# Performance work log

Hardware: AMD Instinct MI355X
Metric: run time of the kernel (lower is better)

Reference implementation:

```python
import jax, jax.numpy as jnp
import numpy as np

N, D, V = 4096, 256, 32000
B, T = 32, 256
U_DECAY, X_DECAY = 0.97, 0.97
EPS = 1e-6


def layernorm_row(z):
    # matches torch: (z - mean) / (std + eps), std with Bessel correction (ddof=1)
    m = jnp.mean(z, axis=-1, keepdims=True)
    s = jnp.std(z, axis=-1, keepdims=True, ddof=1)
    return (z - m) / (s + EPS)


def setup_inputs() -> dict:
    key = jax.random.key(0)
    k1, k2, k3, k4, k5 = jax.random.split(key, 5)
    token_emb = jax.random.normal(k1, (V, D), jnp.float32) / np.float32(np.sqrt(D))
    E = jax.random.normal(k2, (D, N), jnp.float32) / np.float32(np.sqrt(N))
    Dx = jax.random.normal(k3, (N, D), jnp.float32) / np.float32(np.sqrt(D))
    Dy = jax.random.normal(k4, (N, D), jnp.float32) / np.float32(np.sqrt(D))
    idx = jax.random.randint(k5, (B, T), 0, V)
    return {"idx": idx, "token_emb": token_emb, "E": E, "Dx": Dx, "Dy": Dy}


def reference(idx, token_emb, E, Dx, Dy):
    b = idx.shape[0]

    def step(carry, tok):
        x, rho = carry                                   # x: (b,n), rho: (b,d,n)
        v_prev = token_emb[tok]                          # (b,d) embedding gather
        x_t = X_DECAY * x + jax.nn.relu(v_prev @ Dx.T)   # (b,n)
        x_t = x_t / (jnp.sum(jnp.abs(x_t), axis=-1, keepdims=True) + EPS)  # L1 normalize
        a_star = jnp.einsum('bdn,bn->bd', rho, x_t)      # fast-weight readout
        y_t = jax.nn.relu(layernorm_row(a_star) @ Dy.T) * jax.nn.relu(x_t)  # (b,n)
        v_star = layernorm_row(y_t @ E.T)                # (b,d)
        # Hebbian decayed outer-product memory update
        rho = U_DECAY * (rho + jnp.einsum('bd,bn->bdn', layernorm_row(v_prev), x_t))
        return (x_t, rho), v_star

    x0 = jnp.zeros((b, N), jnp.float32)
    rho0 = jnp.zeros((b, D, N), jnp.float32)
    (_, _), vs = jax.lax.scan(step, (x0, rho0), idx.T)   # vs: (T,b,d)
    return jnp.transpose(vs, (1, 0, 2))                  # (b,T,d)
```

## Files before the change

### kernel.cpp

```cpp
#include <hip/hip_runtime.h>
#include <hip/hip_bf16.h>

#define NN 4096
#define DD 256
#define BB 32
#define TT 256
#define EPS 1e-6f
#define DECAY 0.97f
#define LOG2_DECAY -0.043943348f

typedef __hip_bfloat16 bf16;
typedef short short8 __attribute__((ext_vector_type(8)));
typedef float floatx4 __attribute__((ext_vector_type(4)));

__device__ __forceinline__ float bfu2f(short u) {
    return __uint_as_float(((unsigned)(unsigned short)u) << 16);
}
__device__ __forceinline__ short f2bfu(float v) {
    bf16 t = __float2bfloat16(v);
    return *reinterpret_cast<short*>(&t);
}

__device__ __forceinline__ float blk_sum_256(float v, volatile float* s4) {
#pragma unroll
    for (int o = 32; o > 0; o >>= 1) v += __shfl_down(v, o, 64);
    int lane = threadIdx.x & 63, w = threadIdx.x >> 6;
    __syncthreads();
    if (lane == 0) s4[w] = v;
    __syncthreads();
    return s4[0] + s4[1] + s4[2] + s4[3];
}

__device__ __forceinline__ void gl16(const bf16* g, void* l) {
    __builtin_amdgcn_global_load_lds((const __attribute__((address_space(1))) void*)g,
                                     (__attribute__((address_space(3))) void*)l, 16, 0, 0);
}

__device__ __forceinline__ short8 frag(const char* matbase, int row, int c) {
    return *(const short8*)(matbase + row * 128 + (((c) ^ (row & 7)) << 4));
}

__global__ void k_detect(const unsigned short* __restrict__ raw, int* __restrict__ flag) {
    __shared__ int cnt[4];
    int tid = threadIdx.x;
    int bad = 0;
    for (int i = tid; i < 8192; i += 256) {
        unsigned int u = raw[2 * i];
        float v = __uint_as_float(u << 16);
        if (!(fabsf(v) < 1e6f)) bad++;
    }
#pragma unroll
    for (int o = 32; o > 0; o >>= 1) bad += __shfl_down(bad, o, 64);
    int lane = tid & 63, w = tid >> 6;
    if (lane == 0) cnt[w] = bad;
    __syncthreads();
    if (tid == 0) flag[0] = (cnt[0] + cnt[1] + cnt[2] + cnt[3] < 32) ? 1 : 0;
}

__global__ __launch_bounds__(256) void k_convert3(const void* __restrict__ s0,
                                                  const void* __restrict__ s1,
                                                  const void* __restrict__ s2,
                                                  bf16* __restrict__ d0,
                                                  bf16* __restrict__ d1,
                                                  bf16* __restrict__ d2,
                                                  const int* __restrict__ flag) {
    const int per = NN * DD / 8;
    int i = blockIdx.x * 256 + threadIdx.x;
    int m = i / per, j = i % per;
    const void* s = (m == 0) ? s0 : (m == 1) ? s1 : s2;
    bf16* d = (m == 0) ? d0 : (m == 1) ? d1 : d2;
    if (flag[0]) {
        ((uint4*)d)[j] = ((const uint4*)s)[j];
    } else {
        const float4* f = (const float4*)s;
        float4 a = f[2 * j], b = f[2 * j + 1];
        short8 o;
        float va[8] = {a.x, a.y, a.z, a.w, b.x, b.y, b.z, b.w};
#pragma unroll
        for (int k = 0; k < 8; k++) o[k] = f2bfu(va[k]);
        ((short8*)d)[j] = o;
    }
}

__global__ __launch_bounds__(256) void k_gather_ln(const void* __restrict__ emb,
                                                   const int* __restrict__ idx,
                                                   bf16* __restrict__ Vpb,
                                                   bf16* __restrict__ Ub,
                                                   const int* __restrict__ flag) {
    __shared__ float s4[4];
    int r = blockIdx.x, d = threadIdx.x;
    int tok = idx[r];
    long o = (long)tok * DD + d;
    float e = flag[0] ? __bfloat162float(((const bf16*)emb)[o]) : ((const float*)emb)[o];
    Vpb[(long)r * DD + d] = __float2bfloat16(e);
    float m = blk_sum_256(e, s4) * (1.0f / DD);
    float zc = e - m;
    float var = blk_sum_256(zc * zc, s4) * (1.0f / (DD - 1));
    Ub[(long)r * DD + d] = __float2bfloat16(zc / (sqrtf(fmaxf(var, 0.f)) + EPS));
}

__global__ __launch_bounds__(256) void k_transpose(const bf16* __restrict__ Ub,
                                                   bf16* __restrict__ Ut) {
    __shared__ bf16 tile[32][33];
    int b = blockIdx.z;
    int t0 = blockIdx.x * 32, d0 = blockIdx.y * 32;
    const bf16* src = Ub + (long)b * TT * DD;
    bf16* dst = Ut + (long)b * DD * TT;
    int rr = threadIdx.x >> 3, c4 = (threadIdx.x & 7) * 4;
#pragma unroll
    for (int i = 0; i < 4; i++) tile[rr][c4 + i] = src[(long)(t0 + rr) * DD + d0 + c4 + i];
    __syncthreads();
#pragma unroll
    for (int i = 0; i < 4; i++) dst[(long)(d0 + rr) * TT + t0 + c4 + i] = tile[c4 + i][rr];
}

enum { EPI_RELU_BF16 = 0, EPI_RELU_MULX_BF16 = 2 };

template <int EPI>
__global__ __launch_bounds__(256) void k_g128(const bf16* __restrict__ A,
                                              const bf16* __restrict__ B,
                                              bf16* __restrict__ C,
                                              const bf16* __restrict__ Xaux,
                                              float* __restrict__ Wsum) {
    __shared__ __align__(16) char smem[65536];
    const int lda = DD, ldb = DD, ldc = NN;
    int bm = blockIdx.y * 128, bn = blockIdx.x * 128;
    int tid = threadIdx.x, w = tid >> 6, lane = tid & 63;
    int lrow = lane >> 3, lph = lane & 7;
    int rr0 = w * 32;
    int csw = lph ^ lrow;

    floatx4 acc[4][4];
#pragma unroll
    for (int i = 0; i < 4; i++)
#pragma unroll
        for (int j = 0; j < 4; j++) acc[i][j] = (floatx4){0.f, 0.f, 0.f, 0.f};

#define STAGE128(buf, k0)                                                              \
    {                                                                                  \
        char* bb = smem + (buf)*32768;                                                 \
        _Pragma("unroll") for (int j = 0; j < 4; j++) {                                \
            int row = rr0 + j * 8 + lrow;                                              \
            gl16(A + (long)(bm + row) * lda + (k0) + csw * 8,                          \
                 bb + (rr0 + j * 8) * 128 + lane * 16);                                \
            gl16(B + (long)(bn + row) * ldb + (k0) + csw * 8,                          \
                 bb + 16384 + (rr0 + j * 8) * 128 + lane * 16);                        \
        }                                                                              \
    }

    int wm = (w >> 1) * 64, wn = (w & 1) * 64;
    int lm = lane & 15, kh = lane >> 4;

    STAGE128(0, 0);
#pragma unroll
    for (int it = 0; it < 4; it++) {
        __syncthreads();
        if (it < 3) STAGE128((it + 1) & 1, (it + 1) * 64);
        char* Ab = smem + (it & 1) * 32768;
        char* Bb = Ab + 16384;
#pragma unroll
        for (int ks = 0; ks < 2; ks++) {
            int c = ks * 4 + kh;
            short8 af[4], bfr[4];
#pragma unroll
            for (int i = 0; i < 4; i++) af[i] = frag(Ab, wm + i * 16 + lm, c);
#pragma unroll
            for (int j = 0; j < 4; j++) bfr[j] = frag(Bb, wn + j * 16 + lm, c);
#pragma unroll
            for (int i = 0; i < 4; i++)
#pragma unroll
                for (int j = 0; j < 4; j++)
                    acc[i][j] = __builtin_amdgcn_mfma_f32_16x16x32_bf16(af[i], bfr[j], acc[i][j], 0, 0, 0);
        }
    }
#undef STAGE128

    bf16* R = (bf16*)smem;
#pragma unroll
    for (int p = 0; p < 2; p++) {
        __syncthreads();
        if ((w >> 1) == p) {
#pragma unroll
            for (int i = 0; i < 4; i++)
#pragma unroll
                for (int j = 0; j < 4; j++)
#pragma unroll
                    for (int r = 0; r < 4; r++) {
                        int rr = i * 16 + kh * 4 + r;
                        int cc = wn + j * 16 + lm;
                        R[rr * 136 + cc] = __float2bfloat16(fmaxf(acc[i][j][r], 0.f));
                    }
        }
        __syncthreads();
#pragma unroll
        for (int it2 = 0; it2 < 4; it2++) {
            int row_l = it2 * 16 + (tid >> 4);
            int c8 = (tid & 15) * 8;
            short8 vv = *(const short8*)(R + row_l * 136 + c8);
            int gm = bm + p * 64 + row_l;
            long off = (long)gm * ldc + bn + c8;
            if (EPI == EPI_RELU_BF16) {
                *(short8*)(C + off) = vv;
                float s = 0.f;
#pragma unroll
                for (int k = 0; k < 8; k++) s += bfu2f(vv[k]);
#pragma unroll
                for (int o = 8; o > 0; o >>= 1) s += __shfl_down(s, o, 16);
                if ((tid & 15) == 0) atomicAdd(&Wsum[gm], s);
            } else {
                short8 xx = *(const short8*)(Xaux + off);
                short8 oo;
#pragma unroll
                for (int k = 0; k < 8; k++) oo[k] = f2bfu(bfu2f(vv[k]) * fmaxf(bfu2f(xx[k]), 0.f));
                *(short8*)(C + off) = oo;
            }
        }
    }
}

template <int KITERS>
__global__ __launch_bounds__(256) void k_g64x128(const bf16* __restrict__ A, int lda, long sA,
                                                 const bf16* __restrict__ B, int ldb, long sB,
                                                 float* __restrict__ C, int ldc, long sC) {
    __shared__ __align__(16) char smem[49152];
    int z = blockIdx.z;
    A += (long)z * sA;
    B += (long)z * sB;
    long cbase = (long)z * sC;
    int bm = blockIdx.y * 64, bn = blockIdx.x * 128;
    int tid = threadIdx.x, w = tid >> 6, lane = tid & 63;
    int lrow = lane >> 3, lph = lane & 7;
    int csw = lph ^ lrow;

    floatx4 acc[2][4];
#pragma unroll
    for (int i = 0; i < 2; i++)
#pragma unroll
        for (int j = 0; j < 4; j++) acc[i][j] = (floatx4){0.f, 0.f, 0.f, 0.f};

#define STAGE64128(buf, k0)                                                            \
    {                                                                                  \
        char* bb = smem + (buf)*24576;                                                 \
        _Pragma("unroll") for (int j = 0; j < 2; j++) {                                \
            int row = w * 16 + j * 8 + lrow;                                           \
            gl16(A + (long)(bm + row) * lda + (k0) + csw * 8,                          \
                 bb + (w * 16 + j * 8) * 128 + lane * 16);                             \
        }                                                                              \
        _Pragma("unroll") for (int j = 0; j < 4; j++) {                                \
            int row = w * 32 + j * 8 + lrow;                                           \
            gl16(B + (long)(bn + row) * ldb + (k0) + csw * 8,                          \
                 bb + 8192 + (w * 32 + j * 8) * 128 + lane * 16);                      \
        }                                                                              \
    }

    int wm = (w >> 1) * 32, wn = (w & 1) * 64;
    int lm = lane & 15, kh = lane >> 4;

    STAGE64128(0, 0);
    for (int it = 0; it < KITERS; it++) {
        __syncthreads();
        if (it + 1 < KITERS) STAGE64128((it + 1) & 1, (it + 1) * 64);
        char* Ab = smem + (it & 1) * 24576;
        char* Bb = Ab + 8192;
#pragma unroll
        for (int ks = 0; ks < 2; ks++) {
            int c = ks * 4 + kh;
            short8 af[2], bfr[4];
#pragma unroll
            for (int i = 0; i < 2; i++) af[i] = frag(Ab, wm + i * 16 + lm, c);
#pragma unroll
            for (int j = 0; j < 4; j++) bfr[j] = frag(Bb, wn + j * 16 + lm, c);
#pragma unroll
            for (int i = 0; i < 2; i++)
#pragma unroll
                for (int j = 0; j < 4; j++)
                    acc[i][j] = __builtin_amdgcn_mfma_f32_16x16x32_bf16(af[i], bfr[j], acc[i][j], 0, 0, 0);
        }
    }
#undef STAGE64128

#pragma unroll
    for (int i = 0; i < 2; i++)
#pragma unroll
        for (int j = 0; j < 4; j++)
#pragma unroll
            for (int r = 0; r < 4; r++) {
                int gm = bm + wm + i * 16 + kh * 4 + r;
                int gn = bn + wn + j * 16 + lm;
                C[cbase + (long)gm * ldc + gn] = acc[i][j][r];
            }
}

__global__ __launch_bounds__(256) void k_scores(const bf16* __restrict__ X,
                                                bf16* __restrict__ G) {
    __shared__ __align__(16) char smem[32768];
    const int tri_i[10] = {0, 1, 1, 2, 2, 2, 3, 3, 3, 3};
    const int tri_j[10] = {0, 0, 1, 0, 1, 2, 0, 1, 2, 3};
    int z = blockIdx.z;
    const bf16* A = X + (long)z * TT * NN;
    int bm = tri_i[blockIdx.x] * 64, bn = tri_j[blockIdx.x] * 64;
    int tid = threadIdx.x, w = tid >> 6, lane = tid & 63;
    int lrow = lane >> 3, lph = lane & 7;
    int csw = lph ^ lrow;

    floatx4 acc[2][2];
#pragma unroll
    for (int i = 0; i < 2; i++)
#pragma unroll
        for (int j = 0; j < 2; j++) acc[i][j] = (floatx4){0.f, 0.f, 0.f, 0.f};

#define STAGESC(buf, k0)                                                               \
    {                                                                                  \
        char* bb = smem + (buf)*16384;                                                 \
        _Pragma("unroll") for (int j = 0; j < 2; j++) {                                \
            int row = w * 16 + j * 8 + lrow;                                           \
            gl16(A + (long)(bm + row) * NN + (k0) + csw * 8,                           \
                 bb + (w * 16 + j * 8) * 128 + lane * 16);                             \
            gl16(A + (long)(bn + row) * NN + (k0) + csw * 8,                           \
                 bb + 8192 + (w * 16 + j * 8) * 128 + lane * 16);                      \
        }                                                                              \
    }

    int wm = (w >> 1) * 32, wn = (w & 1) * 32;
    int lm = lane & 15, kh = lane >> 4;

    STAGESC(0, 0);
    for (int it = 0; it < 64; it++) {
        __syncthreads();
        if (it < 63) STAGESC((it + 1) & 1, (it + 1) * 64);
        char* Ab = smem + (it & 1) * 16384;
        char* Bb = Ab + 8192;
#pragma unroll
        for (int ks = 0; ks < 2; ks++) {
            int c = ks * 4 + kh;
            short8 af[2], bfr[2];
#pragma unroll
            for (int i = 0; i < 2; i++) af[i] = frag(Ab, wm + i * 16 + lm, c);
#pragma unroll
            for (int j = 0; j < 2; j++) bfr[j] = frag(Bb, wn + j * 16 + lm, c);
#pragma unroll
            for (int i = 0; i < 2; i++)
#pragma unroll
                for (int j = 0; j < 2; j++)
                    acc[i][j] = __builtin_amdgcn_mfma_f32_16x16x32_bf16(af[i], bfr[j], acc[i][j], 0, 0, 0);
        }
    }
#undef STAGESC

    bf16* Gb = G + (long)z * TT * TT;
#pragma unroll
    for (int i = 0; i < 2; i++)
#pragma unroll
        for (int j = 0; j < 2; j++)
#pragma unroll
            for (int r = 0; r < 4; r++) {
                int gt = bm + wm + i * 16 + kh * 4 + r;
                int gs = bn + wn + j * 16 + lm;
                float v = (gs < gt) ? acc[i][j][r] * exp2f((float)(gt - gs) * LOG2_DECAY) : 0.f;
                Gb[(long)gt * TT + gs] = __float2bfloat16(v);
            }
}

__global__ __launch_bounds__(256) void k_scalar_scan(const float* __restrict__ Wsum,
                                                     float* __restrict__ invS) {
    __shared__ float sw[BB * TT];
    for (int i = threadIdx.x; i < BB * TT; i += 256) sw[i] = Wsum[i];
    __syncthreads();
    int b = threadIdx.x;
    if (b < BB) {
        float sig = 0.f;
        for (int t = 0; t < TT; t++) {
            float S = DECAY * sig + sw[b * TT + t];
            float inv = 1.f / (S + EPS);
            invS[b * TT + t] = inv;
            sig = S * inv;
        }
    }
}

__global__ __launch_bounds__(256) void k_colscan(bf16* __restrict__ W,
                                                 const float* __restrict__ invS) {
    __shared__ float sv[TT];
    int b = blockIdx.y;
    sv[threadIdx.x] = invS[b * TT + threadIdx.x];
    __syncthreads();
    int n = blockIdx.x * 256 + threadIdx.x;
    bf16* p = W + (long)b * TT * NN + n;
    float x = 0.f;
    for (int t = 0; t < TT; t += 4) {
        short w0 = *(const short*)(p + (long)t * NN);
        short w1 = *(const short*)(p + (long)(t + 1) * NN);
        short w2 = *(const short*)(p + (long)(t + 2) * NN);
        short w3 = *(const short*)(p + (long)(t + 3) * NN);
        x = (DECAY * x + bfu2f(w0)) * sv[t];
        *(short*)(p + (long)t * NN) = f2bfu(x);
        x = (DECAY * x + bfu2f(w1)) * sv[t + 1];
        *(short*)(p + (long)(t + 1) * NN) = f2bfu(x);
        x = (DECAY * x + bfu2f(w2)) * sv[t + 2];
        *(short*)(p + (long)(t + 2) * NN) = f2bfu(x);
        x = (DECAY * x + bfu2f(w3)) * sv[t + 3];
        *(short*)(p + (long)(t + 3) * NN) = f2bfu(x);
    }
}

__global__ __launch_bounds__(256) void k_ln_rows(const float* __restrict__ Z,
                                                 bf16* __restrict__ O) {
    __shared__ float s4[4];
    long r = blockIdx.x;
    int d = threadIdx.x;
    float z = Z[r * DD + d];
    float m = blk_sum_256(z, s4) * (1.0f / DD);
    float zc = z - m;
    float var = blk_sum_256(zc * zc, s4) * (1.0f / (DD - 1));
    O[r * DD + d] = __float2bfloat16(zc / (sqrtf(fmaxf(var, 0.f)) + EPS));
}

__global__ __launch_bounds__(256) void k_final_ln(const float* __restrict__ Zf,
                                                  void* __restrict__ out,
                                                  const int* __restrict__ flag) {
    __shared__ float s4[4];
    long r = blockIdx.x;
    int d = threadIdx.x;
    long o = r * DD + d;
    float z = Zf[o];
    float m = blk_sum_256(z, s4) * (1.0f / DD);
    float zc = z - m;
    float var = blk_sum_256(zc * zc, s4) * (1.0f / (DD - 1));
    float v = zc / (sqrtf(fmaxf(var, 0.f)) + EPS);
    if (flag[0]) ((bf16*)out)[o] = __float2bfloat16(v);
    else ((float*)out)[o] = v;
}

extern "C" void kernel_launch(void* const* d_in, const int* in_sizes, int n_in,
                              void* d_out, int out_size, void* d_ws, size_t ws_size,
                              hipStream_t stream) {
    const int* idx = (const int*)d_in[0];
    const void* emb = d_in[1];
    const void* E = d_in[2];
    const void* Dx = d_in[3];
    const void* Dy = d_in[4];

    char* base = (char*)d_ws;
    size_t off = 0;
    int* flag = (int*)base; off += 1024;
    bf16* Dxb = (bf16*)(base + off); off += (size_t)NN * DD * 2;
    bf16* Dyb = (bf16*)(base + off); off += (size_t)NN * DD * 2;
    bf16* Eb  = (bf16*)(base + off); off += (size_t)DD * NN * 2;
    bf16* Vpb = (bf16*)(base + off); off += (size_t)BB * TT * DD * 2;
    bf16* Ub  = (bf16*)(base + off); off += (size_t)BB * TT * DD * 2;
    bf16* Ut  = (bf16*)(base + off); off += (size_t)BB * TT * DD * 2;
    float* Wsum = (float*)(base + off); off += (size_t)BB * TT * 4;
    float* invS = (float*)(base + off); off += (size_t)BB * TT * 4;
    bf16* ALNb = (bf16*)(base + off); off += (size_t)BB * TT * DD * 2;
    bf16* G = (bf16*)(base + off); off += (size_t)BB * TT * TT * 2;
    float* Astar = (float*)(base + off); off += (size_t)BB * TT * DD * 4;
    float* Zf = (float*)(base + off); off += (size_t)BB * TT * DD * 4;
    bf16* Xb = (bf16*)(base + off); off += (size_t)BB * TT * NN * 2;

    const int M = BB * TT;

    k_detect<<<1, 256, 0, stream>>>((const unsigned short*)emb, flag);
    k_convert3<<<3 * NN * DD / 8 / 256, 256, 0, stream>>>(Dx, Dy, E, Dxb, Dyb, Eb, flag);
    k_gather_ln<<<M, 256, 0, stream>>>(emb, idx, Vpb, Ub, flag);
    k_transpose<<<dim3(8, 8, BB), 256, 0, stream>>>(Ub, Ut);

    hipMemsetAsync(Wsum, 0, (size_t)M * 4, stream);
    hipMemsetAsync(G, 0, (size_t)BB * TT * TT * 2, stream);

    k_g128<EPI_RELU_BF16><<<dim3(NN / 128, M / 128, 1), 256, 0, stream>>>(
        Vpb, Dxb, Xb, nullptr, Wsum);

    k_scalar_scan<<<1, 256, 0, stream>>>(Wsum, invS);
    k_colscan<<<dim3(NN / 256, BB, 1), 256, 0, stream>>>(Xb, invS);

    k_scores<<<dim3(10, 1, BB), 256, 0, stream>>>(Xb, G);

    k_g64x128<4><<<dim3(DD / 128, TT / 64, BB), 256, 0, stream>>>(
        G, TT, (long)TT * TT, Ut, TT, (long)DD * TT, Astar, DD, (long)TT * DD);
    k_ln_rows<<<M, 256, 0, stream>>>(Astar, ALNb);

    k_g128<EPI_RELU_MULX_BF16><<<dim3(NN / 128, M / 128, 1), 256, 0, stream>>>(
        ALNb, Dyb, Xb, Xb, nullptr);

    k_g64x128<64><<<dim3(DD / 128, M / 64, 1), 256, 0, stream>>>(
        Xb, NN, 0, Eb, NN, 0, Zf, DD, 0);

    k_final_ln<<<M, 256, 0, stream>>>(Zf, d_out, flag);
}
```

Before: 342.0 us.

## Split-K the scores and output GEMMs and shrink k_g128 LDS staging

```diff
diff --git a/kernel.cpp b/kernel.cpp
--- a/kernel.cpp
+++ b/kernel.cpp
@@ -36,7 +36,7 @@
                                      (__attribute__((address_space(3))) void*)l, 16, 0, 0);
 }
 
-__device__ __forceinline__ short8 frag(const char* matbase, int row, int c) {
+__device__ __forceinline__ short8 frag64(const char* matbase, int row, int c) {
     return *(const short8*)(matbase + row * 128 + (((c) ^ (row & 7)) << 4));
 }
 
@@ -122,13 +122,11 @@
                                               bf16* __restrict__ C,
                                               const bf16* __restrict__ Xaux,
                                               float* __restrict__ Wsum) {
-    __shared__ __align__(16) char smem[65536];
+    __shared__ __align__(16) char smem[32768];
     const int lda = DD, ldb = DD, ldc = NN;
     int bm = blockIdx.y * 128, bn = blockIdx.x * 128;
     int tid = threadIdx.x, w = tid >> 6, lane = tid & 63;
-    int lrow = lane >> 3, lph = lane & 7;
-    int rr0 = w * 32;
-    int csw = lph ^ lrow;
+    int srow = lane >> 2, sch = lane & 3;
 
     floatx4 acc[4][4];
 #pragma unroll
@@ -136,44 +134,40 @@
 #pragma unroll
         for (int j = 0; j < 4; j++) acc[i][j] = (floatx4){0.f, 0.f, 0.f, 0.f};
 
-#define STAGE128(buf, k0)                                                              \
+#define STAGE32(buf, k0)                                                               \
     {                                                                                  \
-        char* bb = smem + (buf)*32768;                                                 \
-        _Pragma("unroll") for (int j = 0; j < 4; j++) {                                \
-            int row = rr0 + j * 8 + lrow;                                              \
-            gl16(A + (long)(bm + row) * lda + (k0) + csw * 8,                          \
-                 bb + (rr0 + j * 8) * 128 + lane * 16);                                \
-            gl16(B + (long)(bn + row) * ldb + (k0) + csw * 8,                          \
-                 bb + 16384 + (rr0 + j * 8) * 128 + lane * 16);                        \
+        char* bb = smem + (buf)*16384;                                                 \
+        _Pragma("unroll") for (int j = 0; j < 2; j++) {                                \
+            int row = w * 32 + j * 16 + srow;                                          \
+            gl16(A + (long)(bm + row) * lda + (k0) + sch * 8,                          \
+                 bb + (w * 32 + j * 16) * 64 + lane * 16);                             \
+            gl16(B + (long)(bn + row) * ldb + (k0) + sch * 8,                          \
+                 bb + 8192 + (w * 32 + j * 16) * 64 + lane * 16);                      \
         }                                                                              \
     }
 
     int wm = (w >> 1) * 64, wn = (w & 1) * 64;
     int lm = lane & 15, kh = lane >> 4;
 
-    STAGE128(0, 0);
-#pragma unroll
-    for (int it = 0; it < 4; it++) {
+    STAGE32(0, 0);
+#pragma unroll
+    for (int it = 0; it < 8; it++) {
         __syncthreads();
-        if (it < 3) STAGE128((it + 1) & 1, (it + 1) * 64);
-        char* Ab = smem + (it & 1) * 32768;
-        char* Bb = Ab + 16384;
-#pragma unroll
-        for (int ks = 0; ks < 2; ks++) {
-            int c = ks * 4 + kh;
-            short8 af[4], bfr[4];
-#pragma unroll
-            for (int i = 0; i < 4; i++) af[i] = frag(Ab, wm + i * 16 + lm, c);
-#pragma unroll
-            for (int j = 0; j < 4; j++) bfr[j] = frag(Bb, wn + j * 16 + lm, c);
-#pragma unroll
-            for (int i = 0; i < 4; i++)
-#pragma unroll
-                for (int j = 0; j < 4; j++)
-                    acc[i][j] = __builtin_amdgcn_mfma_f32_16x16x32_bf16(af[i], bfr[j], acc[i][j], 0, 0, 0);
-        }
-    }
-#undef STAGE128
+        if (it < 7) STAGE32((it + 1) & 1, (it + 1) * 32);
+        const char* Ab = smem + (it & 1) * 16384;
+        const char* Bb = Ab + 8192;
+        short8 af[4], bfr[4];
+#pragma unroll
+        for (int i = 0; i < 4; i++) af[i] = *(const short8*)(Ab + (wm + i * 16 + lm) * 64 + kh * 16);
+#pragma unroll
+        for (int j = 0; j < 4; j++) bfr[j] = *(const short8*)(Bb + (wn + j * 16 + lm) * 64 + kh * 16);
+#pragma unroll
+        for (int i = 0; i < 4; i++)
+#pragma unroll
+            for (int j = 0; j < 4; j++)
+                acc[i][j] = __builtin_amdgcn_mfma_f32_16x16x32_bf16(af[i], bfr[j], acc[i][j], 0, 0, 0);
+    }
+#undef STAGE32
 
     bf16* R = (bf16*)smem;
 #pragma unroll
@@ -218,14 +212,16 @@
     }
 }
 
-template <int KITERS>
+template <int KITERS, int KSPLIT>
 __global__ __launch_bounds__(256) void k_g64x128(const bf16* __restrict__ A, int lda, long sA,
                                                  const bf16* __restrict__ B, int ldb, long sB,
                                                  float* __restrict__ C, int ldc, long sC) {
     __shared__ __align__(16) char smem[49152];
     int z = blockIdx.z;
-    A += (long)z * sA;
-    B += (long)z * sB;
+    int bz = z / KSPLIT, ks = z % KSPLIT;
+    A += (long)bz * sA;
+    B += (long)bz * sB;
+    int kbase = ks * KITERS * 64;
     long cbase = (long)z * sC;
     int bm = blockIdx.y * 64, bn = blockIdx.x * 128;
     int tid = threadIdx.x, w = tid >> 6, lane = tid & 63;
@@ -256,20 +252,20 @@
     int wm = (w >> 1) * 32, wn = (w & 1) * 64;
     int lm = lane & 15, kh = lane >> 4;
 
-    STAGE64128(0, 0);
+    STAGE64128(0, kbase);
     for (int it = 0; it < KITERS; it++) {
         __syncthreads();
-        if (it + 1 < KITERS) STAGE64128((it + 1) & 1, (it + 1) * 64);
-        char* Ab = smem + (it & 1) * 24576;
-        char* Bb = Ab + 8192;
-#pragma unroll
-        for (int ks = 0; ks < 2; ks++) {
-            int c = ks * 4 + kh;
+        if (it + 1 < KITERS) STAGE64128((it + 1) & 1, kbase + (it + 1) * 64);
+        const char* Ab = smem + (it & 1) * 24576;
+        const char* Bb = Ab + 8192;
+#pragma unroll
+        for (int ksu = 0; ksu < 2; ksu++) {
+            int c = ksu * 4 + kh;
             short8 af[2], bfr[4];
 #pragma unroll
-            for (int i = 0; i < 2; i++) af[i] = frag(Ab, wm + i * 16 + lm, c);
-#pragma unroll
-            for (int j = 0; j < 4; j++) bfr[j] = frag(Bb, wn + j * 16 + lm, c);
+            for (int i = 0; i < 2; i++) af[i] = frag64(Ab, wm + i * 16 + lm, c);
+#pragma unroll
+            for (int j = 0; j < 4; j++) bfr[j] = frag64(Bb, wn + j * 16 + lm, c);
 #pragma unroll
             for (int i = 0; i < 2; i++)
 #pragma unroll
@@ -292,12 +288,14 @@
 }
 
 __global__ __launch_bounds__(256) void k_scores(const bf16* __restrict__ X,
-                                                bf16* __restrict__ G) {
+                                                float* __restrict__ Gp) {
     __shared__ __align__(16) char smem[32768];
     const int tri_i[10] = {0, 1, 1, 2, 2, 2, 3, 3, 3, 3};
     const int tri_j[10] = {0, 0, 1, 0, 1, 2, 0, 1, 2, 3};
     int z = blockIdx.z;
-    const bf16* A = X + (long)z * TT * NN;
+    int b = z >> 2, ks = z & 3;
+    const bf16* A = X + (long)b * TT * NN;
+    int kbase = ks * 1024;
     int bm = tri_i[blockIdx.x] * 64, bn = tri_j[blockIdx.x] * 64;
     int tid = threadIdx.x, w = tid >> 6, lane = tid & 63;
     int lrow = lane >> 3, lph = lane & 7;
@@ -324,20 +322,20 @@
     int wm = (w >> 1) * 32, wn = (w & 1) * 32;
     int lm = lane & 15, kh = lane >> 4;
 
-    STAGESC(0, 0);
-    for (int it = 0; it < 64; it++) {
+    STAGESC(0, kbase);
+    for (int it = 0; it < 16; it++) {
         __syncthreads();
-        if (it < 63) STAGESC((it + 1) & 1, (it + 1) * 64);
-        char* Ab = smem + (it & 1) * 16384;
-        char* Bb = Ab + 8192;
-#pragma unroll
-        for (int ks = 0; ks < 2; ks++) {
-            int c = ks * 4 + kh;
+        if (it < 15) STAGESC((it + 1) & 1, kbase + (it + 1) * 64);
+        const char* Ab = smem + (it & 1) * 16384;
+        const char* Bb = Ab + 8192;
+#pragma unroll
+        for (int ksu = 0; ksu < 2; ksu++) {
+            int c = ksu * 4 + kh;
             short8 af[2], bfr[2];
 #pragma unroll
-            for (int i = 0; i < 2; i++) af[i] = frag(Ab, wm + i * 16 + lm, c);
-#pragma unroll
-            for (int j = 0; j < 2; j++) bfr[j] = frag(Bb, wn + j * 16 + lm, c);
+            for (int i = 0; i < 2; i++) af[i] = frag64(Ab, wm + i * 16 + lm, c);
+#pragma unroll
+            for (int j = 0; j < 2; j++) bfr[j] = frag64(Bb, wn + j * 16 + lm, c);
 #pragma unroll
             for (int i = 0; i < 2; i++)
 #pragma unroll
@@ -347,7 +345,7 @@
     }
 #undef STAGESC
 
-    bf16* Gb = G + (long)z * TT * TT;
+    float* Gb = Gp + ((long)b * 4 + ks) * 65536;
 #pragma unroll
     for (int i = 0; i < 2; i++)
 #pragma unroll
@@ -356,9 +354,22 @@
             for (int r = 0; r < 4; r++) {
                 int gt = bm + wm + i * 16 + kh * 4 + r;
                 int gs = bn + wn + j * 16 + lm;
-                float v = (gs < gt) ? acc[i][j][r] * exp2f((float)(gt - gs) * LOG2_DECAY) : 0.f;
-                Gb[(long)gt * TT + gs] = __float2bfloat16(v);
+                Gb[(long)gt * TT + gs] = acc[i][j][r];
             }
+}
+
+__global__ __launch_bounds__(256) void k_reduce_mask(const float* __restrict__ Gp,
+                                                     bf16* __restrict__ G) {
+    int r = blockIdx.x;
+    int b = r >> 8, t = r & 255;
+    int s = threadIdx.x;
+    float o = 0.f;
+    if (s < t) {
+        long base = ((long)b * 4) * 65536 + (long)t * 256 + s;
+        float v = Gp[base] + Gp[base + 65536] + Gp[base + 2 * 65536] + Gp[base + 3 * 65536];
+        o = v * exp2f((float)(t - s) * LOG2_DECAY);
+    }
+    G[(long)r * 256 + s] = __float2bfloat16(o);
 }
 
 __global__ __launch_bounds__(256) void k_scalar_scan(const float* __restrict__ Wsum,
@@ -415,14 +426,15 @@
     O[r * DD + d] = __float2bfloat16(zc / (sqrtf(fmaxf(var, 0.f)) + EPS));
 }
 
-__global__ __launch_bounds__(256) void k_final_ln(const float* __restrict__ Zf,
+__global__ __launch_bounds__(256) void k_final_ln(const float* __restrict__ Zp,
                                                   void* __restrict__ out,
                                                   const int* __restrict__ flag) {
     __shared__ float s4[4];
     long r = blockIdx.x;
     int d = threadIdx.x;
+    const long SL = (long)8192 * 256;
     long o = r * DD + d;
-    float z = Zf[o];
+    float z = Zp[o] + Zp[o + SL] + Zp[o + 2 * SL] + Zp[o + 3 * SL];
     float m = blk_sum_256(z, s4) * (1.0f / DD);
     float zc = z - m;
     float var = blk_sum_256(zc * zc, s4) * (1.0f / (DD - 1));
@@ -453,8 +465,9 @@
     float* invS = (float*)(base + off); off += (size_t)BB * TT * 4;
     bf16* ALNb = (bf16*)(base + off); off += (size_t)BB * TT * DD * 2;
     bf16* G = (bf16*)(base + off); off += (size_t)BB * TT * TT * 2;
+    float* Gp = (float*)(base + off); off += (size_t)4 * BB * TT * TT * 4;
+    float* Zp = Gp;
     float* Astar = (float*)(base + off); off += (size_t)BB * TT * DD * 4;
-    float* Zf = (float*)(base + off); off += (size_t)BB * TT * DD * 4;
     bf16* Xb = (bf16*)(base + off); off += (size_t)BB * TT * NN * 2;
 
     const int M = BB * TT;
@@ -465,7 +478,6 @@
     k_transpose<<<dim3(8, 8, BB), 256, 0, stream>>>(Ub, Ut);
 
     hipMemsetAsync(Wsum, 0, (size_t)M * 4, stream);
-    hipMemsetAsync(G, 0, (size_t)BB * TT * TT * 2, stream);
 
     k_g128<EPI_RELU_BF16><<<dim3(NN / 128, M / 128, 1), 256, 0, stream>>>(
         Vpb, Dxb, Xb, nullptr, Wsum);
@@ -473,17 +485,18 @@
     k_scalar_scan<<<1, 256, 0, stream>>>(Wsum, invS);
     k_colscan<<<dim3(NN / 256, BB, 1), 256, 0, stream>>>(Xb, invS);
 
-    k_scores<<<dim3(10, 1, BB), 256, 0, stream>>>(Xb, G);
-
-    k_g64x128<4><<<dim3(DD / 128, TT / 64, BB), 256, 0, stream>>>(
+    k_scores<<<dim3(10, 1, BB * 4), 256, 0, stream>>>(Xb, Gp);
+    k_reduce_mask<<<M, 256, 0, stream>>>(Gp, G);
+
+    k_g64x128<4, 1><<<dim3(DD / 128, TT / 64, BB), 256, 0, stream>>>(
         G, TT, (long)TT * TT, Ut, TT, (long)DD * TT, Astar, DD, (long)TT * DD);
     k_ln_rows<<<M, 256, 0, stream>>>(Astar, ALNb);
 
     k_g128<EPI_RELU_MULX_BF16><<<dim3(NN / 128, M / 128, 1), 256, 0, stream>>>(
         ALNb, Dyb, Xb, Xb, nullptr);
 
-    k_g64x128<64><<<dim3(DD / 128, M / 64, 1), 256, 0, stream>>>(
-        Xb, NN, 0, Eb, NN, 0, Zf, DD, 0);
-
-    k_final_ln<<<M, 256, 0, stream>>>(Zf, d_out, flag);
-}
+    k_g64x128<16, 4><<<dim3(DD / 128, M / 64, 4), 256, 0, stream>>>(
+        Xb, NN, 0, Eb, NN, 0, Zp, DD, (long)M * DD);
+
+    k_final_ln<<<M, 256, 0, stream>>>(Zp, d_out, flag);
+}
```

Measured after the change: 344.5 us. No clear change (+0.7%).
